# Kernel optimization log

Hardware: AMD Instinct MI355X
Metric: run time of the kernel (lower is better)

Reference implementation:

```python
import jax, jax.numpy as jnp
import numpy as np

B, T, D, K = 4, 4096, 384, 64

def setup_inputs() -> dict:
    key = jax.random.key(0)
    k1, k2, k3, k4 = jax.random.split(key, 4)
    x = jax.random.normal(k1, (B, T, D), dtype=jnp.float32)
    # nn.Linear weights stored as (out_features, in_features); y = x @ W.T
    Wk = jax.random.normal(k2, (K, D), dtype=jnp.float32) * (1.0 / np.sqrt(D))
    Wq = jax.random.normal(k3, (K, D), dtype=jnp.float32) * (1.0 / np.sqrt(D))
    Wv = jax.random.normal(k4, (D, D), dtype=jnp.float32) * (1.0 / np.sqrt(D))
    return {"x": x, "Wk": Wk, "Wq": Wq, "Wv": Wv}

def reference(x, Wk, Wq, Wv):
    # x: (B,T,D)
    k = jnp.einsum('btd,kd->btk', x, Wk)   # (B,T,K)
    q = jnp.einsum('btd,kd->btk', x, Wq)   # (B,T,K)
    v = jnp.einsum('btd,ed->bte', x, Wv)   # (B,T,D)
    scores = jnp.einsum('btk,bsk->bts', q, k)  # (B,T,T)
    Tq = x.shape[1]
    causal = jnp.tril(jnp.ones((Tq, Tq), dtype=bool))[None, :, :]
    scores = jnp.where(causal, scores, -jnp.inf)
    w = jax.nn.softmax(scores / jnp.sqrt(jnp.asarray(Wk.shape[0], scores.dtype)), axis=-1)
    return jnp.einsum('bts,bsd->btd', w, v)  # (B,T,D)
```

## Files before the change

kernel.cpp:

```cpp
#include <hip/hip_runtime.h>


#define BB 4
#define TT 4096
#define DD 384

#define OWKA 0
#define OWQA 24576
#define OWVB 49152
#define OYK  196608
#define OYQ  1245184
#define OVT  2293760

#define C_EXP 0.18033688011112042f

typedef __bf16 bf16x8 __attribute__((ext_vector_type(8)));
typedef float f32x16 __attribute__((ext_vector_type(16)));
typedef unsigned short u16x4 __attribute__((ext_vector_type(4)));

__device__ __forceinline__ unsigned short f2bf(float f) {
  unsigned int u = __builtin_bit_cast(unsigned int, f);
  u += 0x7FFFu + ((u >> 16) & 1u);
  return (unsigned short)(u >> 16);
}

__device__ __forceinline__ bf16x8 ldb8(const unsigned short* p) {
  return *reinterpret_cast<const bf16x8*>(p);
}

__global__ __launch_bounds__(256) void convert_w(
    const float* __restrict__ Wk, const float* __restrict__ Wq,
    const float* __restrict__ Wv, unsigned short* __restrict__ ws) {
  int g = blockIdx.x * 256 + threadIdx.x;
  int row = g / 96;
  int fin = (g - row * 96) * 4;
  const float* src;
  unsigned short* dstbase;
  int m;
  if (row < 64)       { src = Wk + row * 384;         dstbase = ws + OWKA; m = row; }
  else if (row < 128) { src = Wq + (row - 64) * 384;  dstbase = ws + OWQA; m = row - 64; }
  else                { src = Wv + (row - 128) * 384; dstbase = ws + OWVB; m = row - 128; }
  float4 f = *reinterpret_cast<const float4*>(src + fin);
  u16x4 o;
  o[0] = f2bf(f.x); o[1] = f2bf(f.y); o[2] = f2bf(f.z); o[3] = f2bf(f.w);
  unsigned short* dst = dstbase + (m >> 5) * 12288 + (fin >> 4) * 512
                        + ((((fin >> 3) & 1) << 5) + (m & 31)) * 8 + (fin & 7);
  *reinterpret_cast<u16x4*>(dst) = o;
}

__global__ __launch_bounds__(512) void proj_fused(
    const float* __restrict__ x, const unsigned short* __restrict__ ws_r,
    unsigned short* __restrict__ Yk, unsigned short* __restrict__ Yq,
    unsigned short* __restrict__ Vt) {
  __shared__ __align__(16) unsigned short xlds[12288];
  int tb2 = blockIdx.x;
  int b = tb2 >> 7;
  int tt = tb2 & 127;
  int tid = threadIdx.x;
  {
    const float* xb = x + tb2 * 12288;
#pragma unroll
    for (int j = 0; j < 6; j++) {
      int v = tid + 512 * j;
      int r = v / 96;
      int fin = (v - r * 96) * 4;
      float4 f = *reinterpret_cast<const float4*>(xb + v * 4);
      u16x4 o;
      o[0] = f2bf(f.x); o[1] = f2bf(f.y); o[2] = f2bf(f.z); o[3] = f2bf(f.w);
      unsigned short* dst = xlds + (fin >> 4) * 512
                            + ((((fin >> 3) & 1) << 5) + r) * 8 + (fin & 7);
      *reinterpret_cast<u16x4*>(dst) = o;
    }
  }
  __syncthreads();
  int wid = tid >> 6, lane = tid & 63;
  int l31 = lane & 31, h8 = lane >> 5;
  const f32x16 fz16 = {};
  if (wid < 2) {
    const unsigned short* Wa = ws_r + (wid ? OWQA : OWKA) + lane * 8;
    unsigned short* Ysel = (wid ? Yq : Yk);
    f32x16 acc[2];
    acc[0] = fz16; acc[1] = fz16;
    for (int ks = 0; ks < 24; ks++) {
      bf16x8 a0 = ldb8(Wa + ks * 512);
      bf16x8 a1 = ldb8(Wa + 12288 + ks * 512);
      bf16x8 b0 = ldb8(xlds + ks * 512 + lane * 8);
      acc[0] = __builtin_amdgcn_mfma_f32_32x32x16_bf16(a0, b0, acc[0], 0, 0, 0);
      acc[1] = __builtin_amdgcn_mfma_f32_32x32x16_bf16(a1, b0, acc[1], 0, 0, 0);
    }
    int tile = b * 128 + tt;
#pragma unroll
    for (int mt = 0; mt < 2; mt++)
#pragma unroll
      for (int rg = 0; rg < 4; rg++) {
        u16x4 o;
#pragma unroll
        for (int i = 0; i < 4; i++) o[i] = f2bf(acc[mt][rg * 4 + i]);
        *reinterpret_cast<u16x4*>(Ysel + tile * 2048 + (mt * 2 + (rg >> 1)) * 512
                                  + (((rg & 1) << 5) + l31) * 8 + 4 * h8) = o;
      }
  } else {
    int vw = wid - 2;
    const unsigned short* Wb = ws_r + OWVB + vw * 2 * 12288 + lane * 8;
    f32x16 acc[2];
    acc[0] = fz16; acc[1] = fz16;
    for (int ks = 0; ks < 24; ks++) {
      bf16x8 a0 = ldb8(xlds + ks * 512 + lane * 8);
      bf16x8 w0 = ldb8(Wb + ks * 512);
      bf16x8 w1 = ldb8(Wb + 12288 + ks * 512);
      acc[0] = __builtin_amdgcn_mfma_f32_32x32x16_bf16(a0, w0, acc[0], 0, 0, 0);
      acc[1] = __builtin_amdgcn_mfma_f32_32x32x16_bf16(a0, w1, acc[1], 0, 0, 0);
    }
    int k128 = tt >> 2;
    int ks0 = (tb2 & 3) * 2;
#pragma unroll
    for (int dt = 0; dt < 2; dt++) {
      int dti = vw * 2 + dt;
      unsigned short* vbase = Vt + ((b * 12 + dti) * 32 + k128) * 4096;
#pragma unroll
      for (int rg = 0; rg < 4; rg++) {
        u16x4 o;
#pragma unroll
        for (int i = 0; i < 4; i++) o[i] = f2bf(acc[dt][rg * 4 + i]);
        int kseg = ks0 + (rg >> 1);
        *reinterpret_cast<u16x4*>(vbase + kseg * 512
                                  + (((rg & 1) << 5) + l31) * 8 + 4 * h8) = o;
      }
    }
  }
}

__global__ __launch_bounds__(256, 2) void flash_attn(
    const unsigned short* __restrict__ Yk, const unsigned short* __restrict__ Yq,
    const unsigned short* __restrict__ Vt, float* __restrict__ out) {
  __shared__ __align__(16) unsigned short pbuf[2][8192];
  __shared__ float lred[4][32];
  int blk = blockIdx.x;
  int xcd = blk & 7;
  int b = xcd >> 1, half = xcd & 1;
  int n = blk >> 3;
  int st = (n < 32) ? (127 - 2 * n - half) : (2 * (n - 32) + half);
  int wid = threadIdx.x >> 6, lane = threadIdx.x & 63;
  int l31 = lane & 31, h8 = lane >> 5;
  const f32x16 fz16 = {};
  const unsigned short* qbase = Yq + (b * 128 + st) * 2048 + lane * 8;
  bf16x8 qf[4];
#pragma unroll
  for (int ks = 0; ks < 4; ks++) qf[ks] = ldb8(qbase + ks * 512);
  f32x16 acc[3];
  acc[0] = fz16; acc[1] = fz16; acc[2] = fz16;
  float psum = 0.f;
  int n128 = (st >> 2) + 1;
  int qrow = st * 32 + l31;
  const unsigned short* kbase = Yk + (b * 128 + wid) * 2048 + lane * 8;
  const unsigned short* vbase = Vt + ((b * 12 + wid * 3) * 32) * 4096 + lane * 8;
#pragma unroll 1
  for (int kb = 0; kb < n128; kb++) {
    const unsigned short* kt = kbase + kb * 8192;
    bf16x8 kf[4];
#pragma unroll
    for (int ks = 0; ks < 4; ks++) kf[ks] = ldb8(kt + ks * 512);
    f32x16 sacc = fz16;
#pragma unroll
    for (int ks = 0; ks < 4; ks++)
      sacc = __builtin_amdgcn_mfma_f32_32x32x16_bf16(kf[ks], qf[ks], sacc, 0, 0, 0);
    int kg0 = kb * 128 + wid * 32 + 4 * h8;
    unsigned short* pw = pbuf[kb & 1];
#pragma unroll
    for (int rg = 0; rg < 4; rg++) {
      u16x4 o;
#pragma unroll
      for (int i = 0; i < 4; i++) {
        int key = kg0 + rg * 8 + i;
        float pv = (key > qrow) ? 0.f : exp2f(sacc[rg * 4 + i] * C_EXP);
        psum += pv;
        o[i] = f2bf(pv);
      }
      int g = wid * 2 + (rg >> 1);
      *reinterpret_cast<u16x4*>(pw + g * 512 + ((rg & 1) * 32 + l31) * 8 + 4 * h8) = o;
    }
    const unsigned short* vt = vbase + kb * 4096;
    bf16x8 vf0[8], vf1[8], vf2[8];
#pragma unroll
    for (int g = 0; g < 8; g++) vf0[g] = ldb8(vt + g * 512);
#pragma unroll
    for (int g = 0; g < 8; g++) vf1[g] = ldb8(vt + 32 * 4096 + g * 512);
#pragma unroll
    for (int g = 0; g < 8; g++) vf2[g] = ldb8(vt + 64 * 4096 + g * 512);
    __syncthreads();
    bf16x8 pf[8];
#pragma unroll
    for (int g = 0; g < 8; g++) pf[g] = ldb8(pw + g * 512 + lane * 8);
#pragma unroll
    for (int g = 0; g < 8; g++) {
      acc[0] = __builtin_amdgcn_mfma_f32_32x32x16_bf16(vf0[g], pf[g], acc[0], 0, 0, 0);
      acc[1] = __builtin_amdgcn_mfma_f32_32x32x16_bf16(vf1[g], pf[g], acc[1], 0, 0, 0);
      acc[2] = __builtin_amdgcn_mfma_f32_32x32x16_bf16(vf2[g], pf[g], acc[2], 0, 0, 0);
    }
  }
  psum += __shfl_xor(psum, 32);
  if (h8 == 0) lred[wid][l31] = psum;
  __syncthreads();
  float lt = lred[0][l31] + lred[1][l31] + lred[2][l31] + lred[3][l31];
  float inv = 1.0f / lt;
  float* ob = out + (b * TT + st * 32 + l31) * DD + wid * 96;
#pragma unroll
  for (int dt = 0; dt < 3; dt++)
#pragma unroll
    for (int rg = 0; rg < 4; rg++) {
      float4 o4;
      o4.x = acc[dt][rg * 4 + 0] * inv; o4.y = acc[dt][rg * 4 + 1] * inv;
      o4.z = acc[dt][rg * 4 + 2] * inv; o4.w = acc[dt][rg * 4 + 3] * inv;
      *reinterpret_cast<float4*>(ob + dt * 32 + rg * 8 + h8 * 4) = o4;
    }
}

extern "C" void kernel_launch(void* const* d_in, const int* in_sizes, int n_in,
                              void* d_out, int out_size, void* d_ws, size_t ws_size,
                              hipStream_t stream) {
  const float* x  = (const float*)d_in[0];
  const float* Wk = (const float*)d_in[1];
  const float* Wq = (const float*)d_in[2];
  const float* Wv = (const float*)d_in[3];
  unsigned short* ws = (unsigned short*)d_ws;
  unsigned short* Yk = ws + OYK;
  unsigned short* Yq = ws + OYQ;
  unsigned short* Vt = ws + OVT;

  convert_w<<<192, 256, 0, stream>>>(Wk, Wq, Wv, ws);
  proj_fused<<<512, 512, 0, stream>>>(x, ws, Yk, Yq, Vt);
  flash_attn<<<512, 256, 0, stream>>>(Yk, Yq, Vt, (float*)d_out);
}
```

Measured before the change: 150.0 us.

## Prefetch next K/V tiles in attention loop and fuse weight conversion into projection

The flash attention loop now loads the next key block's K fragments right after the score MFMAs and the next V fragments after the PV MFMAs. This software-pipelines global loads across iterations instead of stalling at the start of each block, at the cost of extra live registers. The barrier is replaced by an explicit LDS waitcnt plus s_barrier, and output stores become nontemporal. The separate weight-conversion kernel is removed: the projection kernel reads fp32 weights directly and converts them to bf16 on the fly. That saves a launch but re-reads and re-converts the weights in every block.

```diff
diff --git a/kernel.cpp b/kernel.cpp
--- a/kernel.cpp
+++ b/kernel.cpp
@@ -5,9 +5,6 @@
 #define TT 4096
 #define DD 384
 
-#define OWKA 0
-#define OWQA 24576
-#define OWVB 49152
 #define OYK  196608
 #define OYQ  1245184
 #define OVT  2293760
@@ -16,7 +13,9 @@
 
 typedef __bf16 bf16x8 __attribute__((ext_vector_type(8)));
 typedef float f32x16 __attribute__((ext_vector_type(16)));
+typedef float f32x4 __attribute__((ext_vector_type(4)));
 typedef unsigned short u16x4 __attribute__((ext_vector_type(4)));
+typedef unsigned short u16x8 __attribute__((ext_vector_type(8)));
 
 __device__ __forceinline__ unsigned short f2bf(float f) {
   unsigned int u = __builtin_bit_cast(unsigned int, f);
@@ -28,28 +27,18 @@
   return *reinterpret_cast<const bf16x8*>(p);
 }
 
-__global__ __launch_bounds__(256) void convert_w(
-    const float* __restrict__ Wk, const float* __restrict__ Wq,
-    const float* __restrict__ Wv, unsigned short* __restrict__ ws) {
-  int g = blockIdx.x * 256 + threadIdx.x;
-  int row = g / 96;
-  int fin = (g - row * 96) * 4;
-  const float* src;
-  unsigned short* dstbase;
-  int m;
-  if (row < 64)       { src = Wk + row * 384;         dstbase = ws + OWKA; m = row; }
-  else if (row < 128) { src = Wq + (row - 64) * 384;  dstbase = ws + OWQA; m = row - 64; }
-  else                { src = Wv + (row - 128) * 384; dstbase = ws + OWVB; m = row - 128; }
-  float4 f = *reinterpret_cast<const float4*>(src + fin);
-  u16x4 o;
-  o[0] = f2bf(f.x); o[1] = f2bf(f.y); o[2] = f2bf(f.z); o[3] = f2bf(f.w);
-  unsigned short* dst = dstbase + (m >> 5) * 12288 + (fin >> 4) * 512
-                        + ((((fin >> 3) & 1) << 5) + (m & 31)) * 8 + (fin & 7);
-  *reinterpret_cast<u16x4*>(dst) = o;
+__device__ __forceinline__ bf16x8 ldw8(const float* p) {
+  float4 a = *reinterpret_cast<const float4*>(p);
+  float4 b = *reinterpret_cast<const float4*>(p + 4);
+  u16x8 t;
+  t[0] = f2bf(a.x); t[1] = f2bf(a.y); t[2] = f2bf(a.z); t[3] = f2bf(a.w);
+  t[4] = f2bf(b.x); t[5] = f2bf(b.y); t[6] = f2bf(b.z); t[7] = f2bf(b.w);
+  return __builtin_bit_cast(bf16x8, t);
 }
 
 __global__ __launch_bounds__(512) void proj_fused(
-    const float* __restrict__ x, const unsigned short* __restrict__ ws_r,
+    const float* __restrict__ x, const float* __restrict__ Wk,
+    const float* __restrict__ Wq, const float* __restrict__ Wv,
     unsigned short* __restrict__ Yk, unsigned short* __restrict__ Yq,
     unsigned short* __restrict__ Vt) {
   __shared__ __align__(16) unsigned short xlds[12288];
@@ -77,42 +66,45 @@
   int l31 = lane & 31, h8 = lane >> 5;
   const f32x16 fz16 = {};
   if (wid < 2) {
-    const unsigned short* Wa = ws_r + (wid ? OWQA : OWKA) + lane * 8;
+    const float* Ws = wid ? Wq : Wk;
+    const float* w0 = Ws + l31 * DD + h8 * 8;
+    const float* w1 = Ws + (32 + l31) * DD + h8 * 8;
     unsigned short* Ysel = (wid ? Yq : Yk);
-    f32x16 acc[2];
-    acc[0] = fz16; acc[1] = fz16;
+    f32x16 acc0 = fz16, acc1 = fz16;
     for (int ks = 0; ks < 24; ks++) {
-      bf16x8 a0 = ldb8(Wa + ks * 512);
-      bf16x8 a1 = ldb8(Wa + 12288 + ks * 512);
+      bf16x8 a0 = ldw8(w0 + ks * 16);
+      bf16x8 a1 = ldw8(w1 + ks * 16);
       bf16x8 b0 = ldb8(xlds + ks * 512 + lane * 8);
-      acc[0] = __builtin_amdgcn_mfma_f32_32x32x16_bf16(a0, b0, acc[0], 0, 0, 0);
-      acc[1] = __builtin_amdgcn_mfma_f32_32x32x16_bf16(a1, b0, acc[1], 0, 0, 0);
+      acc0 = __builtin_amdgcn_mfma_f32_32x32x16_bf16(a0, b0, acc0, 0, 0, 0);
+      acc1 = __builtin_amdgcn_mfma_f32_32x32x16_bf16(a1, b0, acc1, 0, 0, 0);
     }
     int tile = b * 128 + tt;
+    f32x16 am[2] = {acc0, acc1};
 #pragma unroll
     for (int mt = 0; mt < 2; mt++)
 #pragma unroll
       for (int rg = 0; rg < 4; rg++) {
         u16x4 o;
 #pragma unroll
-        for (int i = 0; i < 4; i++) o[i] = f2bf(acc[mt][rg * 4 + i]);
+        for (int i = 0; i < 4; i++) o[i] = f2bf(am[mt][rg * 4 + i]);
         *reinterpret_cast<u16x4*>(Ysel + tile * 2048 + (mt * 2 + (rg >> 1)) * 512
                                   + (((rg & 1) << 5) + l31) * 8 + 4 * h8) = o;
       }
   } else {
     int vw = wid - 2;
-    const unsigned short* Wb = ws_r + OWVB + vw * 2 * 12288 + lane * 8;
-    f32x16 acc[2];
-    acc[0] = fz16; acc[1] = fz16;
+    const float* w0 = Wv + (vw * 64 + l31) * DD + h8 * 8;
+    const float* w1 = Wv + (vw * 64 + 32 + l31) * DD + h8 * 8;
+    f32x16 acc0 = fz16, acc1 = fz16;
     for (int ks = 0; ks < 24; ks++) {
-      bf16x8 a0 = ldb8(xlds + ks * 512 + lane * 8);
-      bf16x8 w0 = ldb8(Wb + ks * 512);
-      bf16x8 w1 = ldb8(Wb + 12288 + ks * 512);
-      acc[0] = __builtin_amdgcn_mfma_f32_32x32x16_bf16(a0, w0, acc[0], 0, 0, 0);
-      acc[1] = __builtin_amdgcn_mfma_f32_32x32x16_bf16(a0, w1, acc[1], 0, 0, 0);
+      bf16x8 xa = ldb8(xlds + ks * 512 + lane * 8);
+      bf16x8 wv0 = ldw8(w0 + ks * 16);
+      bf16x8 wv1 = ldw8(w1 + ks * 16);
+      acc0 = __builtin_amdgcn_mfma_f32_32x32x16_bf16(xa, wv0, acc0, 0, 0, 0);
+      acc1 = __builtin_amdgcn_mfma_f32_32x32x16_bf16(xa, wv1, acc1, 0, 0, 0);
     }
     int k128 = tt >> 2;
     int ks0 = (tb2 & 3) * 2;
+    f32x16 ad[2] = {acc0, acc1};
 #pragma unroll
     for (int dt = 0; dt < 2; dt++) {
       int dti = vw * 2 + dt;
@@ -121,7 +113,7 @@
       for (int rg = 0; rg < 4; rg++) {
         u16x4 o;
 #pragma unroll
-        for (int i = 0; i < 4; i++) o[i] = f2bf(acc[dt][rg * 4 + i]);
+        for (int i = 0; i < 4; i++) o[i] = f2bf(ad[dt][rg * 4 + i]);
         int kseg = ks0 + (rg >> 1);
         *reinterpret_cast<u16x4*>(vbase + kseg * 512
                                   + (((rg & 1) << 5) + l31) * 8 + 4 * h8) = o;
@@ -154,16 +146,29 @@
   int qrow = st * 32 + l31;
   const unsigned short* kbase = Yk + (b * 128 + wid) * 2048 + lane * 8;
   const unsigned short* vbase = Vt + ((b * 12 + wid * 3) * 32) * 4096 + lane * 8;
+  bf16x8 kf[4];
+#pragma unroll
+  for (int ks = 0; ks < 4; ks++) kf[ks] = ldb8(kbase + ks * 512);
+  bf16x8 vf0[8], vf1[8], vf2[8];
+#pragma unroll
+  for (int g = 0; g < 8; g++) vf0[g] = ldb8(vbase + g * 512);
+#pragma unroll
+  for (int g = 0; g < 8; g++) vf1[g] = ldb8(vbase + 32 * 4096 + g * 512);
+#pragma unroll
+  for (int g = 0; g < 8; g++) vf2[g] = ldb8(vbase + 64 * 4096 + g * 512);
+  asm volatile("" ::: "memory");
 #pragma unroll 1
   for (int kb = 0; kb < n128; kb++) {
-    const unsigned short* kt = kbase + kb * 8192;
-    bf16x8 kf[4];
-#pragma unroll
-    for (int ks = 0; ks < 4; ks++) kf[ks] = ldb8(kt + ks * 512);
     f32x16 sacc = fz16;
 #pragma unroll
     for (int ks = 0; ks < 4; ks++)
       sacc = __builtin_amdgcn_mfma_f32_32x32x16_bf16(kf[ks], qf[ks], sacc, 0, 0, 0);
+    int kn = (kb + 1 < n128) ? kb + 1 : kb;
+    const unsigned short* ktn = kbase + kn * 8192;
+    bf16x8 kfn[4];
+#pragma unroll
+    for (int ks = 0; ks < 4; ks++) kfn[ks] = ldb8(ktn + ks * 512);
+    asm volatile("" ::: "memory");
     int kg0 = kb * 128 + wid * 32 + 4 * h8;
     unsigned short* pw = pbuf[kb & 1];
 #pragma unroll
@@ -179,15 +184,9 @@
       int g = wid * 2 + (rg >> 1);
       *reinterpret_cast<u16x4*>(pw + g * 512 + ((rg & 1) * 32 + l31) * 8 + 4 * h8) = o;
     }
-    const unsigned short* vt = vbase + kb * 4096;
-    bf16x8 vf0[8], vf1[8], vf2[8];
-#pragma unroll
-    for (int g = 0; g < 8; g++) vf0[g] = ldb8(vt + g * 512);
-#pragma unroll
-    for (int g = 0; g < 8; g++) vf1[g] = ldb8(vt + 32 * 4096 + g * 512);
-#pragma unroll
-    for (int g = 0; g < 8; g++) vf2[g] = ldb8(vt + 64 * 4096 + g * 512);
-    __syncthreads();
+    asm volatile("s_waitcnt lgkmcnt(0)" ::: "memory");
+    __builtin_amdgcn_s_barrier();
+    asm volatile("" ::: "memory");
     bf16x8 pf[8];
 #pragma unroll
     for (int g = 0; g < 8; g++) pf[g] = ldb8(pw + g * 512 + lane * 8);
@@ -197,6 +196,16 @@
       acc[1] = __builtin_amdgcn_mfma_f32_32x32x16_bf16(vf1[g], pf[g], acc[1], 0, 0, 0);
       acc[2] = __builtin_amdgcn_mfma_f32_32x32x16_bf16(vf2[g], pf[g], acc[2], 0, 0, 0);
     }
+    const unsigned short* vtn = vbase + kn * 4096;
+#pragma unroll
+    for (int g = 0; g < 8; g++) vf0[g] = ldb8(vtn + g * 512);
+#pragma unroll
+    for (int g = 0; g < 8; g++) vf1[g] = ldb8(vtn + 32 * 4096 + g * 512);
+#pragma unroll
+    for (int g = 0; g < 8; g++) vf2[g] = ldb8(vtn + 64 * 4096 + g * 512);
+    asm volatile("" ::: "memory");
+#pragma unroll
+    for (int ks = 0; ks < 4; ks++) kf[ks] = kfn[ks];
   }
   psum += __shfl_xor(psum, 32);
   if (h8 == 0) lred[wid][l31] = psum;
@@ -208,10 +217,11 @@
   for (int dt = 0; dt < 3; dt++)
 #pragma unroll
     for (int rg = 0; rg < 4; rg++) {
-      float4 o4;
-      o4.x = acc[dt][rg * 4 + 0] * inv; o4.y = acc[dt][rg * 4 + 1] * inv;
-      o4.z = acc[dt][rg * 4 + 2] * inv; o4.w = acc[dt][rg * 4 + 3] * inv;
-      *reinterpret_cast<float4*>(ob + dt * 32 + rg * 8 + h8 * 4) = o4;
+      f32x4 o4;
+      o4[0] = acc[dt][rg * 4 + 0] * inv; o4[1] = acc[dt][rg * 4 + 1] * inv;
+      o4[2] = acc[dt][rg * 4 + 2] * inv; o4[3] = acc[dt][rg * 4 + 3] * inv;
+      __builtin_nontemporal_store(
+          o4, reinterpret_cast<f32x4*>(ob + dt * 32 + rg * 8 + h8 * 4));
     }
 }
 
@@ -227,7 +237,6 @@
   unsigned short* Yq = ws + OYQ;
   unsigned short* Vt = ws + OVT;
 
-  convert_w<<<192, 256, 0, stream>>>(Wk, Wq, Wv, ws);
-  proj_fused<<<512, 512, 0, stream>>>(x, ws, Yk, Yq, Vt);
+  proj_fused<<<512, 512, 0, stream>>>(x, Wk, Wq, Wv, Yk, Yq, Vt);
   flash_attn<<<512, 256, 0, stream>>>(Yk, Yq, Vt, (float*)d_out);
 }
```

After: 177.9 us. 18.5% more time.
